# Performance work log

Measured on AMD Instinct MI355X. Metric: run time of the kernel, lower is better.

Reference implementation:

```python
import jax, jax.numpy as jnp
import numpy as np

G = 32               # sdf grid resolution (grid_size init default)
SCALE_FACTOR = 0.2   # forward default scale_factor
EPS = 1e-12


def setup_inputs() -> dict:
    key = jax.random.key(0)
    k1, k2 = jax.random.split(key)
    H, V, F = 2, 778, 1538  # two hands, MANO topology
    vertices = jax.random.normal(k1, (H, V, 3), dtype=jnp.float32)
    faces = jax.random.randint(k2, (F, 3), 0, V, dtype=jnp.int32)
    return {"vertices": vertices, "faces": faces}


def _sdiv(n, d):
    return n / jnp.where(jnp.abs(d) < EPS, EPS, d)


def _point_tri_dist2(p, a, b, c):
    # p: [P,1,3]; a,b,c: [1,F,3] -> squared distance [P,F] (Ericson closest-point)
    ab = b - a; ac = c - a; ap = p - a
    d1 = jnp.sum(ab * ap, -1); d2 = jnp.sum(ac * ap, -1)
    bp = p - b; d3 = jnp.sum(ab * bp, -1); d4 = jnp.sum(ac * bp, -1)
    cp = p - c; d5 = jnp.sum(ab * cp, -1); d6 = jnp.sum(ac * cp, -1)
    vc = d1 * d4 - d3 * d2
    vb = d5 * d2 - d1 * d6
    va = d3 * d6 - d5 * d4
    denom = va + vb + vc
    v_in = _sdiv(vb, denom); w_in = _sdiv(vc, denom)
    res = a + ab * v_in[..., None] + ac * w_in[..., None]  # face interior
    # edge BC
    cond = ((va <= 0) & ((d4 - d3) >= 0) & ((d5 - d6) >= 0))[..., None]
    w = _sdiv(d4 - d3, (d4 - d3) + (d5 - d6))[..., None]
    res = jnp.where(cond, b + (c - b) * w, res)
    # edge AC
    cond = ((vb <= 0) & (d2 >= 0) & (d6 <= 0))[..., None]
    w = _sdiv(d2, d2 - d6)[..., None]
    res = jnp.where(cond, a + ac * w, res)
    # edge AB
    cond = ((vc <= 0) & (d1 >= 0) & (d3 <= 0))[..., None]
    w = _sdiv(d1, d1 - d3)[..., None]
    res = jnp.where(cond, a + ab * w, res)
    # vertex regions (highest precedence)
    res = jnp.where(((d6 >= 0) & (d5 <= d6))[..., None], jnp.broadcast_to(c, res.shape), res)
    res = jnp.where(((d3 >= 0) & (d4 <= d3))[..., None], jnp.broadcast_to(b, res.shape), res)
    res = jnp.where(((d1 <= 0) & (d2 <= 0))[..., None], jnp.broadcast_to(a, res.shape), res)
    return jnp.sum((p - res) ** 2, -1)


def _inside(p, a, b, c):
    # parity of +x ray intersections (Moller-Trumbore with dir = (1,0,0))
    e1 = b - a; e2 = c - a
    det = e1[..., 1] * (-e2[..., 2]) + e1[..., 2] * e2[..., 1]  # dot(e1, cross(dir,e2))
    inv = _sdiv(1.0, det)
    s = p - a
    u = (s[..., 1] * (-e2[..., 2]) + s[..., 2] * e2[..., 1]) * inv
    q = jnp.cross(s, e1)
    v = q[..., 0] * inv                # dot(dir, q)
    t = jnp.sum(e2 * q, -1) * inv
    hit = (jnp.abs(det) > 1e-9) & (u >= 0) & (u <= 1) & (v >= 0) & (u + v <= 1) & (t > 0)
    return (jnp.sum(hit.astype(jnp.int32), axis=-1) % 2) == 1


def _sdf_grid(tri):
    # tri: [F,3,3] scaled triangles -> phi [G,G,G] laid out [z,y,x] (grid_sample DHW)
    a = tri[None, :, 0]; b = tri[None, :, 1]; c = tri[None, :, 2]
    lin = jnp.linspace(-1.0, 1.0, G, dtype=tri.dtype)
    zz, yy, xx = jnp.meshgrid(lin, lin, lin, indexing='ij')
    pts = jnp.stack([xx, yy, zz], -1).reshape(G, G * G, 3)  # chunk over z-slabs

    def slab(ps):
        p = ps[:, None, :]
        d2 = jnp.min(_point_tri_dist2(p, a, b, c), axis=1)
        ins = _inside(p, a, b, c)
        return jnp.where(ins, jnp.sqrt(jnp.maximum(d2, 0.0)), 0.0)

    return jax.lax.map(slab, pts).reshape(G, G, G)


def _trilinear(phi, coords):
    # grid_sample(align_corners=True, padding_mode='zeros'), coords [N,3] in xyz order
    g = G - 1
    f = (coords + 1.0) * 0.5 * g
    fx, fy, fz = f[:, 0], f[:, 1], f[:, 2]
    x0f = jnp.floor(fx); y0f = jnp.floor(fy); z0f = jnp.floor(fz)
    wx = fx - x0f; wy = fy - y0f; wz = fz - z0f
    x0 = x0f.astype(jnp.int32); y0 = y0f.astype(jnp.int32); z0 = z0f.astype(jnp.int32)

    def corner(zi, yi, xi, w):
        valid = (zi >= 0) & (zi <= g) & (yi >= 0) & (yi <= g) & (xi >= 0) & (xi <= g)
        val = phi[jnp.clip(zi, 0, g), jnp.clip(yi, 0, g), jnp.clip(xi, 0, g)]
        return jnp.where(valid, val, 0.0) * w

    out = (corner(z0, y0, x0, (1 - wz) * (1 - wy) * (1 - wx))
           + corner(z0, y0, x0 + 1, (1 - wz) * (1 - wy) * wx)
           + corner(z0, y0 + 1, x0, (1 - wz) * wy * (1 - wx))
           + corner(z0, y0 + 1, x0 + 1, (1 - wz) * wy * wx)
           + corner(z0 + 1, y0, x0, wz * (1 - wy) * (1 - wx))
           + corner(z0 + 1, y0, x0 + 1, wz * (1 - wy) * wx)
           + corner(z0 + 1, y0 + 1, x0, wz * wy * (1 - wx))
           + corner(z0 + 1, y0 + 1, x0 + 1, wz * wy * wx))
    return out


def reference(vertices, faces):
    H = vertices.shape[0]
    bmin = vertices.min(axis=1)   # [H,3]
    bmax = vertices.max(axis=1)
    center = jax.lax.stop_gradient(((bmin + bmax) * 0.5)[:, None, :])           # [H,1,3]
    scale = jax.lax.stop_gradient(
        ((1.0 + SCALE_FACTOR) * 0.5 * (bmax - bmin).max(-1))[:, None, None])    # [H,1,1]
    v_scaled = jax.lax.stop_gradient((vertices - center) / scale)
    tris = v_scaled[:, faces]                                                    # [H,F,3,3]
    phi = jax.lax.stop_gradient(jax.vmap(_sdf_grid)(tris))                       # [H,G,G,G]
    i = 1  # hardcoded loop 'for i in [1]' in the source
    coords = ((vertices - center[i][None]) / scale[i][None]).reshape(-1, 3)
    phi_val = _trilinear(phi[i], coords).reshape(H, -1)
    weights = jnp.ones((H, 1), dtype=vertices.dtype).at[i, 0].set(0.0)
    loss = jnp.sum(weights * phi_val) / (H ** 2)
    return loss
```

## Files before the change

### kernel.cpp

```cpp
#include <hip/hip_runtime.h>
#include <math.h>

#define NNODE 32768
#define NTHR  256
#define NCH   8
#define MAXF8 224

__device__ __forceinline__ float rguard(float d) {
    float dd = (fabsf(d) < 1e-12f) ? 1e-12f : d;
    return __builtin_amdgcn_rcpf(dd);
}

__device__ __forceinline__ void cell_of(float px, float py, float pz,
                                        int& x0, int& y0, int& z0,
                                        float& wx, float& wy, float& wz) {
#pragma clang fp contract(off)
    float fx = (px + 1.0f) * 0.5f * 31.0f;
    float fy = (py + 1.0f) * 0.5f * 31.0f;
    float fz = (pz + 1.0f) * 0.5f * 31.0f;
    float x0f = floorf(fx), y0f = floorf(fy), z0f = floorf(fz);
    wx = fx - x0f; wy = fy - y0f; wz = fz - z0f;
    x0 = (int)fmaxf(fminf(x0f, 33.0f), -2.0f);
    y0 = (int)fmaxf(fminf(y0f, 33.0f), -2.0f);
    z0 = (int)fmaxf(fminf(z0f, 33.0f), -2.0f);
}

__device__ __forceinline__ void bbox_of(const float* __restrict__ verts, int V,
                                        float& ocx, float& ocy, float& ocz,
                                        float& osc) {
#pragma clang fp contract(off)
    const float* v1 = verts + (size_t)V * 3;
    float mn[3] = {1e30f, 1e30f, 1e30f};
    float mx[3] = {-1e30f, -1e30f, -1e30f};
    for (int i = threadIdx.x; i < V; i += blockDim.x) {
        for (int c = 0; c < 3; ++c) {
            float val = v1[i * 3 + c];
            mn[c] = fminf(mn[c], val);
            mx[c] = fmaxf(mx[c], val);
        }
    }
    for (int off = 32; off >= 1; off >>= 1) {
        for (int c = 0; c < 3; ++c) {
            mn[c] = fminf(mn[c], __shfl_down(mn[c], off));
            mx[c] = fmaxf(mx[c], __shfl_down(mx[c], off));
        }
    }
    __shared__ float smn[16][3], smx[16][3];
    int wv = threadIdx.x >> 6, lane = threadIdx.x & 63;
    if (lane == 0)
        for (int c = 0; c < 3; ++c) { smn[wv][c] = mn[c]; smx[wv][c] = mx[c]; }
    __syncthreads();
    const int nw = (int)blockDim.x >> 6;
    float ext = -1e30f, cc[3];
    for (int c = 0; c < 3; ++c) {
        float lo = 1e30f, hi = -1e30f;
        for (int w = 0; w < nw; ++w) {
            lo = fminf(lo, smn[w][c]);
            hi = fmaxf(hi, smx[w][c]);
        }
        cc[c] = (lo + hi) * 0.5f;
        ext = fmaxf(ext, hi - lo);
    }
    ocx = cc[0]; ocy = cc[1]; ocz = cc[2];
    osc = (1.0f + 0.2f) * 0.5f * ext;
    __syncthreads();
}

__device__ __forceinline__ void tri_node(
        float ax, float ay, float az, float abx, float aby, float abz,
        float acx, float acy, float acz, float inv, float det,
        float dbb, float dbc, float dcc,
        float px, float py, float pz, float& mind2, int& h) {
    float apx = px - ax, apy = py - ay, apz = pz - az;
    {
#pragma clang fp contract(fast)
        float d1 = abx * apx + aby * apy + abz * apz;
        float d2 = acx * apx + acy * apy + acz * apz;
        float d3 = d1 - dbb;
        float d4 = d2 - dbc;
        float d5 = d1 - dbc;
        float d6 = d2 - dcc;
        float vc = d1 * d4 - d3 * d2;
        float vb = d5 * d2 - d1 * d6;
        float va = d3 * d6 - d5 * d4;
        float denom = va + vb + vc;
        float rd = rguard(denom);
        float v_in = vb * rd, w_in = vc * rd;
        float rx = ax + abx * v_in + acx * w_in;
        float ry = ay + aby * v_in + acy * w_in;
        float rz = az + abz * v_in + acz * w_in;
        if (va <= 0.0f && (d4 - d3) >= 0.0f && (d5 - d6) >= 0.0f) {
            float w2 = (d4 - d3) * rguard((d4 - d3) + (d5 - d6));
            rx = ax + abx + (acx - abx) * w2;
            ry = ay + aby + (acy - aby) * w2;
            rz = az + abz + (acz - abz) * w2;
        }
        if (vb <= 0.0f && d2 >= 0.0f && d6 <= 0.0f) {
            float w2 = d2 * rguard(d2 - d6);
            rx = ax + acx * w2; ry = ay + acy * w2; rz = az + acz * w2;
        }
        if (vc <= 0.0f && d1 >= 0.0f && d3 <= 0.0f) {
            float w2 = d1 * rguard(d1 - d3);
            rx = ax + abx * w2; ry = ay + aby * w2; rz = az + abz * w2;
        }
        if (d6 >= 0.0f && d5 <= d6) { rx = ax + acx; ry = ay + acy; rz = az + acz; }
        if (d3 >= 0.0f && d4 <= d3) { rx = ax + abx; ry = ay + aby; rz = az + abz; }
        if (d1 <= 0.0f && d2 <= 0.0f) { rx = ax; ry = ay; rz = az; }
        float ddx = px - rx, ddy = py - ry, ddz = pz - rz;
        mind2 = fminf(mind2, ddx * ddx + ddy * ddy + ddz * ddz);
    }
    {
#pragma clang fp contract(off)
        float u = (apy * (-acz) + apz * acy) * inv;
        float qx = apy * abz - apz * aby;
        float qy = apz * abx - apx * abz;
        float qz = apx * aby - apy * abx;
        float v = qx * inv;
        float tt = (acx * qx + acy * qy + acz * qz) * inv;
        h += (fabsf(det) > 1e-9f && u >= 0.0f && u <= 1.0f && v >= 0.0f &&
              (u + v) <= 1.0f && tt > 0.0f) ? 1 : 0;
    }
}

__global__ void __launch_bounds__(NTHR) k_setup(
        const float* __restrict__ verts, const int* __restrict__ faces,
        float* __restrict__ tri, unsigned int* __restrict__ d2b,
        int* __restrict__ hits, int* __restrict__ cnt, int* __restrict__ list,
        int V, int F) {
    float cx0, cy0, cz0, sc;
    bbox_of(verts, V, cx0, cy0, cz0, sc);
    const int b = (int)blockIdx.x, tid = threadIdx.x;

    for (int t = b * NTHR + tid; t < NNODE; t += (int)gridDim.x * NTHR) {
        d2b[t] = 0xFFFFFFFFu;
        hits[t] = 0;
    }

    if (b == 0) {
        __shared__ unsigned bm[NNODE / 32];
        __shared__ int scnt[NTHR];
        for (int k = 0; k < 4; ++k) bm[tid * 4 + k] = 0u;
        __syncthreads();
        for (int i = tid; i < V; i += NTHR) {
#pragma clang fp contract(off)
            float px = (verts[i * 3 + 0] - cx0) / sc;
            float py = (verts[i * 3 + 1] - cy0) / sc;
            float pz = (verts[i * 3 + 2] - cz0) / sc;
            int x0, y0, z0; float wx, wy, wz;
            cell_of(px, py, pz, x0, y0, z0, wx, wy, wz);
            for (int k = 0; k < 8; ++k) {
                int zi = z0 + ((k >> 2) & 1), yi = y0 + ((k >> 1) & 1),
                    xi = x0 + (k & 1);
                if ((unsigned)zi < 32u && (unsigned)yi < 32u && (unsigned)xi < 32u) {
                    int node = (zi * 32 + yi) * 32 + xi;
                    atomicOr(&bm[node >> 5], 1u << (node & 31));
                }
            }
        }
        __syncthreads();
        unsigned w0 = bm[tid * 4 + 0], w1 = bm[tid * 4 + 1],
                 w2 = bm[tid * 4 + 2], w3 = bm[tid * 4 + 3];
        int c = __popc(w0) + __popc(w1) + __popc(w2) + __popc(w3);
        scnt[tid] = c;
        __syncthreads();
        for (int off = 1; off < NTHR; off <<= 1) {
            int v_ = (tid >= off) ? scnt[tid - off] : 0;
            __syncthreads();
            scnt[tid] += v_;
            __syncthreads();
        }
        if (tid == NTHR - 1) cnt[0] = scnt[NTHR - 1];
        int off = scnt[tid] - c;
        unsigned wsv[4] = {w0, w1, w2, w3};
        for (int k = 0; k < 4; ++k) {
            unsigned w = wsv[k];
            int basebit = (tid * 4 + k) * 32;
            while (w) {
                int bb = __ffs(w) - 1;
                list[off++] = basebit + bb;
                w &= w - 1;
            }
        }
    } else {
        int f = (b - 1) * NTHR + tid;
        if (f < F) {
#pragma clang fp contract(off)
            const float* v1 = verts + (size_t)V * 3;
            int i0 = faces[f * 3 + 0], i1 = faces[f * 3 + 1], i2 = faces[f * 3 + 2];
            float ax = (v1[i0 * 3 + 0] - cx0) / sc, ay = (v1[i0 * 3 + 1] - cy0) / sc,
                  az = (v1[i0 * 3 + 2] - cz0) / sc;
            float bx = (v1[i1 * 3 + 0] - cx0) / sc, by = (v1[i1 * 3 + 1] - cy0) / sc,
                  bz = (v1[i1 * 3 + 2] - cz0) / sc;
            float cx = (v1[i2 * 3 + 0] - cx0) / sc, cy = (v1[i2 * 3 + 1] - cy0) / sc,
                  cz = (v1[i2 * 3 + 2] - cz0) / sc;
            float abx = bx - ax, aby = by - ay, abz = bz - az;
            float acx = cx - ax, acy = cy - ay, acz = cz - az;
            float det = aby * (-acz) + abz * acy;
            float dd = (fabsf(det) < 1e-12f) ? 1e-12f : det;
            float inv = 1.0f / dd;
            float* r = tri + (size_t)f * 16;
            r[0] = ax;  r[1] = ay;  r[2] = az;
            r[3] = abx; r[4] = aby; r[5] = abz;
            r[6] = acx; r[7] = acy; r[8] = acz;
            r[9] = inv; r[10] = det;
            r[11] = abx * abx + aby * aby + abz * abz;
            r[12] = abx * acx + aby * acy + abz * acz;
            r[13] = acx * acx + acy * acy + acz * acz;
            r[14] = 0.0f; r[15] = 0.0f;
        }
    }
}

__global__ void __launch_bounds__(NTHR) k_main(
        const float* __restrict__ tri, const int* __restrict__ list,
        const int* __restrict__ cnt, unsigned int* __restrict__ d2b,
        int* __restrict__ hits, int F) {
    const int n = cnt[0];
    const int group = (int)blockIdx.x >> 3;
    if (group * 4 >= n) return;
    const int c = (int)blockIdx.x & 7;
    const int F8 = (F + NCH - 1) / NCH;
    const int cbase = c * F8;
    const int tn = min(F8, F - cbase);
    if (tn <= 0) return;

    __shared__ float s[14][MAXF8];
    const int tid = threadIdx.x, lane = tid & 63;
    for (int j = tid; j < tn; j += NTHR) {
        const float4* g = (const float4*)(tri + (size_t)(cbase + j) * 16);
        float4 r0 = g[0], r1 = g[1], r2 = g[2], r3 = g[3];
        s[0][j] = r0.x;  s[1][j] = r0.y;  s[2][j] = r0.z;  s[3][j] = r0.w;
        s[4][j] = r1.x;  s[5][j] = r1.y;  s[6][j] = r1.z;  s[7][j] = r1.w;
        s[8][j] = r2.x;  s[9][j] = r2.y;  s[10][j] = r2.z; s[11][j] = r2.w;
        s[12][j] = r3.x; s[13][j] = r3.y;
    }
    __syncthreads();

    const int idx = group * 4 + (tid >> 6);
    const int node = (idx < n) ? list[idx] : -1;
    float px = 0, py = 0, pz = 0;
    if (node >= 0) {
#pragma clang fp contract(off)
        px = (float)((double)(node & 31) * (2.0 / 31.0) - 1.0);
        py = (float)((double)((node >> 5) & 31) * (2.0 / 31.0) - 1.0);
        pz = (float)((double)(node >> 10) * (2.0 / 31.0) - 1.0);
    }
    float m = 1e30f;
    int h = 0;
    if (node >= 0) {
        for (int mi = 0; mi * 64 < tn; ++mi) {
            int j = lane + mi * 64;
            if (j < tn) {
                tri_node(s[0][j], s[1][j], s[2][j], s[3][j], s[4][j], s[5][j],
                         s[6][j], s[7][j], s[8][j], s[9][j], s[10][j],
                         s[11][j], s[12][j], s[13][j], px, py, pz, m, h);
            }
        }
    }
    for (int off = 32; off >= 1; off >>= 1) {
        m = fminf(m, __shfl_xor(m, off));
        h += __shfl_xor(h, off);
    }
    if (lane == 0 && node >= 0) {
        atomicMin(d2b + node, __float_as_uint(m));
        atomicAdd(hits + node, h);
    }
}

__global__ void k_sum(const float* __restrict__ verts,
                      const unsigned int* __restrict__ d2b, const int* __restrict__ hits,
                      float* __restrict__ out, int V) {
    float cx, cy, cz, sc;
    bbox_of(verts, V, cx, cy, cz, sc);
    {
#pragma clang fp contract(off)
        __shared__ float sm[1024];
        const int tid = threadIdx.x;
        float val = 0.0f;
        for (int i = tid; i < V; i += 1024) {
            float px = (verts[i * 3 + 0] - cx) / sc;
            float py = (verts[i * 3 + 1] - cy) / sc;
            float pz = (verts[i * 3 + 2] - cz) / sc;
            int x0, y0, z0; float wx, wy, wz;
            cell_of(px, py, pz, x0, y0, z0, wx, wy, wz);
            auto corner = [&](int zi, int yi, int xi, float w) -> float {
#pragma clang fp contract(off)
                bool valid = (zi >= 0) && (zi <= 31) && (yi >= 0) && (yi <= 31) &&
                             (xi >= 0) && (xi <= 31);
                int zc = min(max(zi, 0), 31);
                int yc = min(max(yi, 0), 31);
                int xc = min(max(xi, 0), 31);
                int idx = (zc * 32 + yc) * 32 + xc;
                float vv = (hits[idx] & 1)
                               ? sqrtf(fmaxf(__uint_as_float(d2b[idx]), 0.0f))
                               : 0.0f;
                return valid ? vv * w : 0.0f;
            };
            val += corner(z0, y0, x0, (1.0f - wz) * (1.0f - wy) * (1.0f - wx))
                 + corner(z0, y0, x0 + 1, (1.0f - wz) * (1.0f - wy) * wx)
                 + corner(z0, y0 + 1, x0, (1.0f - wz) * wy * (1.0f - wx))
                 + corner(z0, y0 + 1, x0 + 1, (1.0f - wz) * wy * wx)
                 + corner(z0 + 1, y0, x0, wz * (1.0f - wy) * (1.0f - wx))
                 + corner(z0 + 1, y0, x0 + 1, wz * (1.0f - wy) * wx)
                 + corner(z0 + 1, y0 + 1, x0, wz * wy * (1.0f - wx))
                 + corner(z0 + 1, y0 + 1, x0 + 1, wz * wy * wx);
        }
        sm[tid] = val;
        __syncthreads();
        for (int ss = 512; ss >= 1; ss >>= 1) {
            if (tid < ss) sm[tid] += sm[tid + ss];
            __syncthreads();
        }
        if (tid == 0) out[0] = sm[0] * 0.25f;
    }
}

extern "C" void kernel_launch(void* const* d_in, const int* in_sizes, int n_in,
                              void* d_out, int out_size, void* d_ws, size_t ws_size,
                              hipStream_t stream) {
    const float* verts = (const float*)d_in[0];
    const int* faces = (const int*)d_in[1];
    float* out = (float*)d_out;
    float* ws = (float*)d_ws;

    int V = in_sizes[0] / 6;
    int F = in_sizes[1] / 3;

    float* tri = ws;
    unsigned int* d2b = (unsigned int*)(tri + 16 * (size_t)F);
    int* hits = (int*)(d2b + NNODE);
    int* cnt = hits + NNODE;
    int* list = cnt + 1;

    int nrec = (F + NTHR - 1) / NTHR;
    int nmax = 8 * V; if (nmax > NNODE) nmax = NNODE;
    int nblk_main = ((nmax + 3) / 4) * NCH;

    k_setup<<<1 + nrec, NTHR, 0, stream>>>(verts, faces, tri, d2b, hits, cnt, list,
                                           V, F);
    k_main<<<nblk_main, NTHR, 0, stream>>>(tri, list, cnt, d2b, hits, F);
    k_sum<<<1, 1024, 0, stream>>>(verts, d2b, hits, out, V);
}
```

Baseline: 47.55 us.

## Use persistent 2D grid: face chunks in x, strided node groups in y

k_main previously launched one block per (4-node group, one of 8 face chunks), with the grid sized from the worst-case node count 8*V, so many blocks exited early. It now launches a fixed 2D grid: x covers 128-face chunks loaded into shared memory once per block, and y holds 160 blocks that grid-stride over node groups. Each face tile in shared memory is reused across many nodes, and early-exiting blocks are no longer launched. In exchange there are more atomic updates per node (about 13 chunks instead of 8), and the total block count is fixed regardless of how many nodes are active.

```diff
diff --git a/kernel.cpp b/kernel.cpp
--- a/kernel.cpp
+++ b/kernel.cpp
@@ -3,8 +3,8 @@
 
 #define NNODE 32768
 #define NTHR  256
-#define NCH   8
-#define MAXF8 224
+#define CHUNK 128
+#define GY    160
 
 __device__ __forceinline__ float rguard(float d) {
     float dd = (fabsf(d) < 1e-12f) ? 1e-12f : d;
@@ -215,39 +215,36 @@
         const float* __restrict__ tri, const int* __restrict__ list,
         const int* __restrict__ cnt, unsigned int* __restrict__ d2b,
         int* __restrict__ hits, int F) {
+    __shared__ float s[14][CHUNK];
+    const int tid = threadIdx.x, lane = tid & 63, wv = tid >> 6;
+    const int cbase = (int)blockIdx.x * CHUNK;
+    const int tn = min(CHUNK, F - cbase);
+
+    if (tid < tn) {
+        const float4* g = (const float4*)(tri + (size_t)(cbase + tid) * 16);
+        float4 r0 = g[0], r1 = g[1], r2 = g[2], r3 = g[3];
+        s[0][tid] = r0.x;  s[1][tid] = r0.y;  s[2][tid] = r0.z;  s[3][tid] = r0.w;
+        s[4][tid] = r1.x;  s[5][tid] = r1.y;  s[6][tid] = r1.z;  s[7][tid] = r1.w;
+        s[8][tid] = r2.x;  s[9][tid] = r2.y;  s[10][tid] = r2.z; s[11][tid] = r2.w;
+        s[12][tid] = r3.x; s[13][tid] = r3.y;
+    }
+    __syncthreads();
+
     const int n = cnt[0];
-    const int group = (int)blockIdx.x >> 3;
-    if (group * 4 >= n) return;
-    const int c = (int)blockIdx.x & 7;
-    const int F8 = (F + NCH - 1) / NCH;
-    const int cbase = c * F8;
-    const int tn = min(F8, F - cbase);
-    if (tn <= 0) return;
-
-    __shared__ float s[14][MAXF8];
-    const int tid = threadIdx.x, lane = tid & 63;
-    for (int j = tid; j < tn; j += NTHR) {
-        const float4* g = (const float4*)(tri + (size_t)(cbase + j) * 16);
-        float4 r0 = g[0], r1 = g[1], r2 = g[2], r3 = g[3];
-        s[0][j] = r0.x;  s[1][j] = r0.y;  s[2][j] = r0.z;  s[3][j] = r0.w;
-        s[4][j] = r1.x;  s[5][j] = r1.y;  s[6][j] = r1.z;  s[7][j] = r1.w;
-        s[8][j] = r2.x;  s[9][j] = r2.y;  s[10][j] = r2.z; s[11][j] = r2.w;
-        s[12][j] = r3.x; s[13][j] = r3.y;
-    }
-    __syncthreads();
-
-    const int idx = group * 4 + (tid >> 6);
-    const int node = (idx < n) ? list[idx] : -1;
-    float px = 0, py = 0, pz = 0;
-    if (node >= 0) {
-#pragma clang fp contract(off)
-        px = (float)((double)(node & 31) * (2.0 / 31.0) - 1.0);
-        py = (float)((double)((node >> 5) & 31) * (2.0 / 31.0) - 1.0);
-        pz = (float)((double)(node >> 10) * (2.0 / 31.0) - 1.0);
-    }
-    float m = 1e30f;
-    int h = 0;
-    if (node >= 0) {
+    const int ngroups = (n + 3) >> 2;
+    for (int g = (int)blockIdx.y; g < ngroups; g += (int)gridDim.y) {
+        const int idx = g * 4 + wv;
+        if (idx >= n) continue;
+        const int node = list[idx];
+        float px, py, pz;
+        {
+#pragma clang fp contract(off)
+            px = (float)((double)(node & 31) * (2.0 / 31.0) - 1.0);
+            py = (float)((double)((node >> 5) & 31) * (2.0 / 31.0) - 1.0);
+            pz = (float)((double)(node >> 10) * (2.0 / 31.0) - 1.0);
+        }
+        float m = 1e30f;
+        int h = 0;
         for (int mi = 0; mi * 64 < tn; ++mi) {
             int j = lane + mi * 64;
             if (j < tn) {
@@ -256,14 +253,14 @@
                          s[11][j], s[12][j], s[13][j], px, py, pz, m, h);
             }
         }
-    }
-    for (int off = 32; off >= 1; off >>= 1) {
-        m = fminf(m, __shfl_xor(m, off));
-        h += __shfl_xor(h, off);
-    }
-    if (lane == 0 && node >= 0) {
-        atomicMin(d2b + node, __float_as_uint(m));
-        atomicAdd(hits + node, h);
+        for (int off = 32; off >= 1; off >>= 1) {
+            m = fminf(m, __shfl_xor(m, off));
+            h += __shfl_xor(h, off);
+        }
+        if (lane == 0) {
+            atomicMin(d2b + node, __float_as_uint(m));
+            atomicAdd(hits + node, h);
+        }
     }
 }
 
@@ -333,11 +330,10 @@
     int* list = cnt + 1;
 
     int nrec = (F + NTHR - 1) / NTHR;
-    int nmax = 8 * V; if (nmax > NNODE) nmax = NNODE;
-    int nblk_main = ((nmax + 3) / 4) * NCH;
+    int nch = (F + CHUNK - 1) / CHUNK;
 
     k_setup<<<1 + nrec, NTHR, 0, stream>>>(verts, faces, tri, d2b, hits, cnt, list,
                                            V, F);
-    k_main<<<nblk_main, NTHR, 0, stream>>>(tri, list, cnt, d2b, hits, F);
+    k_main<<<dim3(nch, GY), NTHR, 0, stream>>>(tri, list, cnt, d2b, hits, F);
     k_sum<<<1, 1024, 0, stream>>>(verts, d2b, hits, out, V);
 }
```

After: 47.97 us. No clear change (+0.9%).
